# Kernel tuning notes

Measured on AMD Instinct MI355X. Metric: run time of the kernel, lower is better.

The kernel has to match this reference:

```python
import jax, jax.numpy as jnp
import numpy as np

FEAT, HW, C, M, U, B = 2048, 14, 20, 64, 128, 4


def _grid_sample_one(img, grid):
    # img: [M, H, W]; grid: [H, W, 2] normalized coords (x, y), align_corners=True, zero padding
    H, W = img.shape[-2], img.shape[-1]
    gx = (grid[..., 0] + 1.0) * 0.5 * (W - 1)
    gy = (grid[..., 1] + 1.0) * 0.5 * (H - 1)
    x0 = jnp.floor(gx).astype(jnp.int32); x1 = x0 + 1
    y0 = jnp.floor(gy).astype(jnp.int32); y1 = y0 + 1

    def gather(yi, xi):
        valid = (yi >= 0) & (yi < H) & (xi >= 0) & (xi < W)
        yc = jnp.clip(yi, 0, H - 1); xc = jnp.clip(xi, 0, W - 1)
        return img[:, yc, xc] * valid.astype(img.dtype)  # [M, H, W]

    w00 = (x1 - gx) * (y1 - gy); w01 = (gx - x0) * (y1 - gy)
    w10 = (x1 - gx) * (gy - y0); w11 = (gx - x0) * (gy - y0)
    return (gather(y0, x0) * w00 + gather(y0, x1) * w01 +
            gather(y1, x0) * w10 + gather(y1, x1) * w11)


def setup_inputs() -> dict:
    key = jax.random.key(0)
    ks = jax.random.split(key, 5)
    x = jax.random.normal(ks[0], (B, FEAT, HW, HW), jnp.float32)
    W_parcel = jax.random.normal(ks[1], (C, M, FEAT), jnp.float32) * 0.02
    W_stn = jax.random.normal(ks[2], (C, 6, M * (HW // 2) ** 2), jnp.float32) * 1e-3
    b_stn = jnp.tile(jnp.array([1.0, 0.0, 0.0, 0.0, 1.0, 0.0], jnp.float32), (C, 1))
    Wg = jax.random.normal(ks[3], (C, C - 1, U, 2 * M), jnp.float32) * 0.02
    w_phi = jax.random.normal(ks[4], (1, U), jnp.float32) * 0.05
    b_phi = jnp.zeros((1,), jnp.float32)
    return {"x": x, "W_parcel": W_parcel, "W_stn": W_stn, "b_stn": b_stn,
            "Wg": Wg, "w_phi": w_phi, "b_phi": b_phi}


def reference(x, W_parcel, W_stn, b_stn, Wg, w_phi, b_phi):
    b, _, H, W = x.shape
    # per-class 1x1 conv parcels: [B, C, M, H, W]
    x_tmp = jnp.einsum('bfhw,cmf->bcmhw', x, W_parcel)
    # relu + 2x2 maxpool -> [B, C, M, 7, 7]
    pooled = jax.nn.relu(x_tmp).reshape(b, C, M, H // 2, 2, W // 2, 2).max(axis=(4, 6))
    flat = pooled.reshape(b, C, M * (H // 2) * (W // 2))
    theta = (jnp.einsum('bck,cjk->bcj', flat, W_stn) + b_stn).reshape(b, C, 2, 3)
    # affine grid (align_corners=True): base[h, w] = [x_norm, y_norm, 1]
    xs = jnp.linspace(-1.0, 1.0, W); ys = jnp.linspace(-1.0, 1.0, H)
    base = jnp.stack(jnp.broadcast_arrays(xs[None, :], ys[:, None], jnp.ones((H, W))), -1)
    grid = jnp.einsum('bcij,hwj->bchwi', theta, base)  # [B, C, H, W, 2]
    # STN sampling of the pre-relu parcel maps
    x_obj = jax.vmap(jax.vmap(_grid_sample_one))(x_tmp, grid)  # [B, C, M, H, W]
    # pairwise relation: relu(Wa[i,j] x_obj[i] + Wb[i,j] x_obj[j]) summed over j != i
    jidx = jnp.asarray(np.array([[k for k in range(C) if k != c] for c in range(C)]))
    Wa, Wb = Wg[..., :M], Wg[..., M:]
    A = jnp.einsum('ckum,bcmhw->bckuhw', Wa, x_obj)
    Bp = jnp.einsum('ckum,bckmhw->bckuhw', Wb, x_obj[:, jidx])
    rel = jax.nn.relu(A + Bp).sum(axis=2)          # [B, C, U, H, W]
    rel_mean = rel.mean(axis=(-2, -1))             # [B, C, U]  (adaptive avg pool 1x1)
    out = jnp.einsum('bcu,ou->bco', rel_mean, w_phi)[..., 0] + b_phi  # [B, C]
    return out
```

## Files before the change

kernel.cpp:

```cpp
#include <hip/hip_runtime.h>

#define FEAT 2048
#define HWD 14
#define NPIX 196
#define C_CLS 20
#define M_DIM 64
#define U_DIM 128
#define B_SZ 4
#define K_REL 19
#define NPOOL 49

typedef __attribute__((ext_vector_type(8))) short bf16x8s;
typedef __attribute__((ext_vector_type(8))) unsigned short ushort8v;
typedef __attribute__((ext_vector_type(4))) float f32x4;
typedef __attribute__((ext_vector_type(4))) unsigned int uint4v;

__device__ inline unsigned short f2bf(float f) {
    unsigned u = __builtin_bit_cast(unsigned, f);
    unsigned r = (u + 0x7FFF + ((u >> 16) & 1)) >> 16;
    return (unsigned short)r;
}

__global__ __launch_bounds__(256) void prep_kernel(
        const float* __restrict__ x, const float* __restrict__ Wp,
        const float* __restrict__ Wg,
        unsigned short* __restrict__ xts, unsigned short* __restrict__ Awp,
        unsigned short* __restrict__ Awg) {
    __shared__ unsigned short SM[128 * 136];
    const int blk = blockIdx.x;
    const int tid = threadIdx.x;
    const int lane = tid & 63, wv = tid >> 6;
    const int l15 = lane & 15, lq = lane >> 4;

    if (blk < 128) {
        unsigned short (*T)[210] = (unsigned short (*)[210])SM;
        const int b = blk >> 5;
        const int s = blk & 31;
        const float* xb = x + ((size_t)b * FEAT + s * 64) * NPIX;
        for (int i = tid; i < 64 * NPIX; i += 256) {
            int kk = i / NPIX, hw = i - kk * NPIX;
            T[kk][hw] = f2bf(xb[(size_t)kk * NPIX + hw]);
        }
        __syncthreads();
        unsigned short* ob = xts + ((size_t)(b * 32 + s)) * 1664 * 8;
        for (int i = tid; i < 1664; i += 256) {
            int ch = i / 208, row = i - ch * 208;
            ushort8v o;
#pragma unroll
            for (int j = 0; j < 8; j++)
                o[j] = (row < NPIX) ? T[ch * 8 + j][row] : (unsigned short)0;
            *(ushort8v*)(ob + (size_t)i * 8) = o;
        }
    } else if (blk < 288) {
        unsigned short (*TP)[264] = (unsigned short (*)[264])SM;
        const int p = blk - 128;
        const int c = p >> 3, kc = p & 7;
        const float* wsrc = Wp + ((size_t)c * M_DIM) * FEAT + kc * 256;
#pragma unroll
        for (int it = 0; it < 16; it++) {
            int i4 = tid + it * 256;
            int m = i4 >> 6, c4 = i4 & 63;
            float4 v = *(const float4*)(wsrc + (size_t)m * FEAT + c4 * 4);
            TP[m][c4 * 4 + 0] = f2bf(v.x);
            TP[m][c4 * 4 + 1] = f2bf(v.y);
            TP[m][c4 * 4 + 2] = f2bf(v.z);
            TP[m][c4 * 4 + 3] = f2bf(v.w);
        }
        __syncthreads();
#pragma unroll
        for (int fr = 0; fr < 8; fr++) {
            int ss = wv;
            int fi = fr;
            int rt = fi >> 1, f = fi & 1;
            int m = rt * 16 + l15;
            int kl = ss * 64 + f * 32 + lq * 8;
            bf16x8s vfrag = *(const bf16x8s*)(&TP[m][kl]);
            int s = kc * 4 + ss;
            *(bf16x8s*)(Awp + (((size_t)(c * 32 + s) * 8 + fi) * 64 + lane) * 8) = vfrag;
        }
    } else {
        unsigned short (*TG)[136] = (unsigned short (*)[136])SM;
        const int ck = blk - 288;
        const float* gsrc = Wg + (size_t)ck * U_DIM * 128;
#pragma unroll
        for (int it = 0; it < 16; it++) {
            int i4 = tid + it * 256;
            int u = i4 >> 5, c4 = i4 & 31;
            float4 v = *(const float4*)(gsrc + (size_t)u * 128 + c4 * 4);
            TG[u][c4 * 4 + 0] = f2bf(v.x);
            TG[u][c4 * 4 + 1] = f2bf(v.y);
            TG[u][c4 * 4 + 2] = f2bf(v.z);
            TG[u][c4 * 4 + 3] = f2bf(v.w);
        }
        __syncthreads();
#pragma unroll
        for (int fr = 0; fr < 8; fr++) {
            int fi = fr;
            int ut = fi >> 2, ks = fi & 3;
            int u = wv * 32 + ut * 16 + l15;
            int mm = ks * 32 + lq * 8;
            bf16x8s vfrag = *(const bf16x8s*)(&TG[u][mm]);
            *(bf16x8s*)(Awg + (((size_t)(ck * 4 + wv) * 8 + fi) * 64 + lane) * 8) = vfrag;
        }
    }
}

__global__ __launch_bounds__(512) void gemmphase_kernel(
        const unsigned short* __restrict__ xts,
        const unsigned short* __restrict__ Awp,
        const float* __restrict__ Wstn,
        const float* __restrict__ bstn,
        unsigned short* __restrict__ x_objT) {
    __shared__ __align__(16) char smem[78336];
    float* xs     = (float*)smem;
    float* pooled = (float*)(smem + 53504);
    float* red    = (float*)(smem + 66048);

    const int c = blockIdx.x, b = blockIdx.y;
    const int tid = threadIdx.x;
    const int lane = tid & 63, wv = tid >> 6;
    const int l15 = lane & 15, lq = lane >> 4;
    const int kh = wv >> 2;
    const int cg = wv & 3;
    const int t0 = (cg == 0) ? 0 : (3 * cg + 1);
    const int nt = (cg == 0) ? 4 : 3;

    const unsigned short* xsrc = xts + (size_t)b * 32 * 1664 * 8;
    const unsigned short* asrc = Awp + (size_t)c * 256 * 64 * 8;
    const int s0 = kh * 16;

    bf16x8s A0[8], A1[8], B0[8], B1[8];
    auto aload = [&](int s, bf16x8s (&A)[8]) {
#pragma unroll
        for (int fi = 0; fi < 8; fi++)
            A[fi] = *(const bf16x8s*)(asrc + (((size_t)s * 8 + fi) * 64 + lane) * 8);
    };
    auto bload = [&](int s, bf16x8s (&B)[8]) {
#pragma unroll
        for (int q = 0; q < 4; q++) {
            if (q < nt) {
#pragma unroll
                for (int f = 0; f < 2; f++)
                    B[q * 2 + f] = *(const bf16x8s*)(xsrc +
                        ((size_t)s * 1664 + (f * 4 + lq) * 208 + (t0 + q) * 16 + l15) * 8);
            }
        }
    };

    f32x4 acc[4][4];
#pragma unroll
    for (int q = 0; q < 4; q++)
#pragma unroll
        for (int rt = 0; rt < 4; rt++) acc[q][rt] = (f32x4){0.f, 0.f, 0.f, 0.f};

    auto compute = [&](bf16x8s (&A)[8], bf16x8s (&B)[8]) {
#pragma unroll
        for (int q = 0; q < 4; q++) {
            if (q < nt) {
#pragma unroll
                for (int rt = 0; rt < 4; rt++)
#pragma unroll
                    for (int f = 0; f < 2; f++)
                        acc[q][rt] = __builtin_amdgcn_mfma_f32_16x16x32_bf16(
                            A[rt * 2 + f], B[q * 2 + f], acc[q][rt], 0, 0, 0);
            }
        }
    };

    aload(s0, A0); bload(s0, B0);
#pragma unroll
    for (int sp = 0; sp < 8; sp++) {
        aload(s0 + 2 * sp + 1, A1); bload(s0 + 2 * sp + 1, B1);
        compute(A0, B0);
        if (sp < 7) { aload(s0 + 2 * sp + 2, A0); bload(s0 + 2 * sp + 2, B0); }
        compute(A1, B1);
    }

    if (kh == 0) {
#pragma unroll
        for (int q = 0; q < 4; q++) {
            if (q < nt) {
                int tt = t0 + q;
#pragma unroll
                for (int rt = 0; rt < 4; rt++)
#pragma unroll
                    for (int r = 0; r < 4; r++)
                        xs[(rt * 16 + lq * 4 + r) * 209 + tt * 16 + l15] = acc[q][rt][r];
            }
        }
    }
    __syncthreads();
    if (kh == 1) {
#pragma unroll
        for (int q = 0; q < 4; q++) {
            if (q < nt) {
                int tt = t0 + q;
#pragma unroll
                for (int rt = 0; rt < 4; rt++)
#pragma unroll
                    for (int r = 0; r < 4; r++)
                        xs[(rt * 16 + lq * 4 + r) * 209 + tt * 16 + l15] += acc[q][rt][r];
            }
        }
    }
    __syncthreads();

    for (int i = tid; i < 3136; i += 512) {
        int m = i / NPOOL, p = i - m * NPOOL;
        int ph = p / 7, pw = p - ph * 7;
        const float* bp = &xs[m * 209 + ph * 2 * HWD + pw * 2];
        float v = fmaxf(fmaxf(bp[0], bp[1]), fmaxf(bp[HWD], bp[HWD + 1]));
        pooled[i] = fmaxf(v, 0.f);
    }
    __syncthreads();

    float sj[6] = {0, 0, 0, 0, 0, 0};
#pragma unroll
    for (int it = 0; it < 7; it++) {
        int kk = tid + it * 512;
        if (kk < 3136) {
            float f = pooled[kk];
#pragma unroll
            for (int j = 0; j < 6; j++)
                sj[j] += f * Wstn[((size_t)c * 6 + j) * 3136 + kk];
        }
    }
#pragma unroll
    for (int j = 0; j < 6; j++) red[j * 512 + tid] = sj[j];
    __syncthreads();
    for (int off = 256; off > 0; off >>= 1) {
        if (tid < off) {
#pragma unroll
            for (int j = 0; j < 6; j++)
                red[j * 512 + tid] += red[j * 512 + tid + off];
        }
        __syncthreads();
    }
    float th[6];
#pragma unroll
    for (int j = 0; j < 6; j++) th[j] = red[j * 512] + bstn[c * 6 + j];

    unsigned short* obase = x_objT + ((size_t)(b * C_CLS + c) * 208) * 64;
    for (int i = tid; i < 12 * 64; i += 512)
        obase[(size_t)(NPIX + i / 64) * 64 + (i & 63)] = 0;

    const int m = tid & 63;
    const int hwg = tid >> 6;
    unsigned short* ob = obase + m;
    const float* xrow = &xs[m * 209];
    for (int it = 0; it < 25; it++) {
        int hw = hwg + it * 8;
        if (hw >= NPIX) break;
        int h = hw / HWD, w = hw - h * HWD;
        float fx = -1.f + w * (2.f / 13.f);
        float fy = -1.f + h * (2.f / 13.f);
        float gxn = th[0] * fx + th[1] * fy + th[2];
        float gyn = th[3] * fx + th[4] * fy + th[5];
        float gx = (gxn + 1.f) * 0.5f * (HWD - 1);
        float gy = (gyn + 1.f) * 0.5f * (HWD - 1);
        float x0f = floorf(gx), y0f = floorf(gy);
        int x0 = (int)x0f, y0 = (int)y0f;
        int x1 = x0 + 1, y1 = y0 + 1;
        auto gat = [&](int yi, int xi) -> float {
            bool v = (yi >= 0) & (yi < HWD) & (xi >= 0) & (xi < HWD);
            int yc = min(max(yi, 0), HWD - 1);
            int xc = min(max(xi, 0), HWD - 1);
            return v ? xrow[yc * HWD + xc] : 0.f;
        };
        float xw1 = (float)x1 - gx, xw0 = gx - (float)x0;
        float yw1 = (float)y1 - gy, yw0 = gy - (float)y0;
        float val = gat(y0, x0) * xw1 * yw1 + gat(y0, x1) * xw0 * yw1 +
                    gat(y1, x0) * xw1 * yw0 + gat(y1, x1) * xw0 * yw0;
        ob[(size_t)hw * 64] = f2bf(val);
    }
}

#define MP 136
__global__ __launch_bounds__(256) void relation_mfma_kernel(
        const unsigned short* __restrict__ x_objT,
        const unsigned short* __restrict__ Awg,
        float* __restrict__ partial) {
    __shared__ unsigned short Xs[208 * MP];
    const int k = blockIdx.x;
    const int c = blockIdx.y;
    const int b = blockIdx.z;
    const int kj = (k < c) ? k : k + 1;
    const int tid = threadIdx.x;
    const int lane = tid & 63;
    const int wv = tid >> 6;
    const int l15 = lane & 15;
    const int lq = lane >> 4;

    bf16x8s AF[2][4];
    const unsigned short* ab = Awg + (((size_t)(c * K_REL + k) * 4 + wv) * 8 * 64) * 8;
#pragma unroll
    for (int ut = 0; ut < 2; ut++)
#pragma unroll
        for (int ks = 0; ks < 4; ks++)
            AF[ut][ks] = *(const bf16x8s*)(ab + ((size_t)(ut * 4 + ks) * 64 + lane) * 8);

    const unsigned short* xc = x_objT + ((size_t)(b * C_CLS + c)) * 208 * 64;
    const unsigned short* xk = x_objT + ((size_t)(b * C_CLS + kj)) * 208 * 64;
#pragma unroll
    for (int it = 0; it < 13; it++) {
        int i = tid + it * 256;
        int hw = i >> 4, ch = i & 15;
        const unsigned short* src = (ch < 8 ? xc : xk) + (size_t)hw * 64 + (ch & 7) * 8;
        *(uint4v*)(&Xs[hw * MP + ch * 8]) = *(const uint4v*)src;
    }
    __syncthreads();

    float csum[2][4];
#pragma unroll
    for (int ut = 0; ut < 2; ut++)
#pragma unroll
        for (int r = 0; r < 4; r++) csum[ut][r] = 0.f;

    for (int t = 0; t < 13; t++) {
        bf16x8s BF[4];
#pragma unroll
        for (int ks = 0; ks < 4; ks++)
            BF[ks] = *(const bf16x8s*)(&Xs[(t * 16 + l15) * MP + ks * 32 + lq * 8]);
        f32x4 acc0 = {0.f, 0.f, 0.f, 0.f}, acc1 = {0.f, 0.f, 0.f, 0.f};
#pragma unroll
        for (int ks = 0; ks < 4; ks++) {
            acc0 = __builtin_amdgcn_mfma_f32_16x16x32_bf16(AF[0][ks], BF[ks], acc0, 0, 0, 0);
            acc1 = __builtin_amdgcn_mfma_f32_16x16x32_bf16(AF[1][ks], BF[ks], acc1, 0, 0, 0);
        }
#pragma unroll
        for (int r = 0; r < 4; r++) {
            csum[0][r] += fmaxf(acc0[r], 0.f);
            csum[1][r] += fmaxf(acc1[r], 0.f);
        }
    }
#pragma unroll
    for (int mask = 1; mask < 16; mask <<= 1) {
#pragma unroll
        for (int ut = 0; ut < 2; ut++)
#pragma unroll
            for (int r = 0; r < 4; r++)
                csum[ut][r] += __shfl_xor(csum[ut][r], mask, 64);
    }
    if (l15 == 0) {
        float* pp = partial + (((size_t)b * C_CLS + c) * K_REL + k) * U_DIM;
#pragma unroll
        for (int ut = 0; ut < 2; ut++)
#pragma unroll
            for (int r = 0; r < 4; r++)
                pp[wv * 32 + ut * 16 + lq * 4 + r] = csum[ut][r];
    }
}

__global__ __launch_bounds__(128) void final_kernel(
        const float* __restrict__ partial, const float* __restrict__ wphi,
        const float* __restrict__ bphi, float* __restrict__ out) {
    int bc = blockIdx.x;
    int u = threadIdx.x;
    float s = 0.f;
    for (int k = 0; k < K_REL; k++)
        s += partial[((size_t)bc * K_REL + k) * U_DIM + u];
    s *= wphi[u];
    __shared__ float red[128];
    red[u] = s;
    __syncthreads();
    for (int off = 64; off > 0; off >>= 1) {
        if (u < off) red[u] += red[u + off];
        __syncthreads();
    }
    if (u == 0) out[bc] = red[0] / (float)NPIX + bphi[0];
}

extern "C" void kernel_launch(void* const* d_in, const int* in_sizes, int n_in,
                              void* d_out, int out_size, void* d_ws, size_t ws_size,
                              hipStream_t stream) {
    const float* x    = (const float*)d_in[0];
    const float* Wp   = (const float*)d_in[1];
    const float* Wstn = (const float*)d_in[2];
    const float* bstn = (const float*)d_in[3];
    const float* Wg   = (const float*)d_in[4];
    const float* wphi = (const float*)d_in[5];
    const float* bphi = (const float*)d_in[6];
    float* out = (float*)d_out;
    char* wsb = (char*)d_ws;

    unsigned short* xts    = (unsigned short*)(wsb);
    unsigned short* Awp    = (unsigned short*)(wsb + 3407872);
    unsigned short* Awg    = (unsigned short*)(wsb + 8650752);
    unsigned short* x_objT = (unsigned short*)(wsb + 21102592);
    float* partial         = (float*)(wsb + 23232512);

    prep_kernel<<<668, 256, 0, stream>>>(x, Wp, Wg, xts, Awp, Awg);
    gemmphase_kernel<<<dim3(C_CLS, B_SZ), 512, 0, stream>>>(xts, Awp, Wstn, bstn, x_objT);
    relation_mfma_kernel<<<dim3(K_REL, C_CLS, B_SZ), 256, 0, stream>>>(x_objT, Awg, partial);
    final_kernel<<<80, 128, 0, stream>>>(partial, wphi, bphi, out);
}
```

Measured before the change: 65.02 us.

## Fuse final reduction into relation kernel via last-block atomic counter; swizzle block ids

Removes the separate final_kernel launch. Each relation block bumps a per-(b,c) atomic counter, and the last block to finish sums the partials and writes the output. Counters are zeroed in prep_kernel. Block indices in the gemmphase and relation kernels are remapped with an XCD-style swizzle (stride 8) so related work lands on the same chiplet and shares L2. This adds threadfence and atomic overhead and a small serial tail in the last block.

Result: slower. 194.6 us (+199.4%).

```diff
diff --git a/kernel.cpp b/kernel.cpp
--- a/kernel.cpp
+++ b/kernel.cpp
@@ -25,12 +25,14 @@
         const float* __restrict__ x, const float* __restrict__ Wp,
         const float* __restrict__ Wg,
         unsigned short* __restrict__ xts, unsigned short* __restrict__ Awp,
-        unsigned short* __restrict__ Awg) {
+        unsigned short* __restrict__ Awg, int* __restrict__ cnt) {
     __shared__ unsigned short SM[128 * 136];
     const int blk = blockIdx.x;
     const int tid = threadIdx.x;
     const int lane = tid & 63, wv = tid >> 6;
     const int l15 = lane & 15, lq = lane >> 4;
+
+    if (blk == 0 && tid < 80) cnt[tid] = 0;
 
     if (blk < 128) {
         unsigned short (*T)[210] = (unsigned short (*)[210])SM;
@@ -116,7 +118,8 @@
     float* pooled = (float*)(smem + 53504);
     float* red    = (float*)(smem + 66048);
 
-    const int c = blockIdx.x, b = blockIdx.y;
+    const int flat = (blockIdx.x & 7) * 10 + (blockIdx.x >> 3);
+    const int c = flat % C_CLS, b = flat / C_CLS;
     const int tid = threadIdx.x;
     const int lane = tid & 63, wv = tid >> 6;
     const int l15 = lane & 15, lq = lane >> 4;
@@ -279,11 +282,17 @@
 __global__ __launch_bounds__(256) void relation_mfma_kernel(
         const unsigned short* __restrict__ x_objT,
         const unsigned short* __restrict__ Awg,
-        float* __restrict__ partial) {
+        float* __restrict__ partial,
+        const float* __restrict__ wphi, const float* __restrict__ bphi,
+        int* __restrict__ cnt, float* __restrict__ out) {
     __shared__ unsigned short Xs[208 * MP];
-    const int k = blockIdx.x;
-    const int c = blockIdx.y;
-    const int b = blockIdx.z;
+    __shared__ int lastFlag;
+    __shared__ float redf[128];
+    const int swz = (blockIdx.x & 7) * 190 + (blockIdx.x >> 3);
+    const int k = swz % K_REL;
+    const int bc = swz / K_REL;
+    const int c = bc % C_CLS;
+    const int b = bc / C_CLS;
     const int kj = (k < c) ? k : k + 1;
     const int tid = threadIdx.x;
     const int lane = tid & 63;
@@ -342,32 +351,36 @@
                 csum[ut][r] += __shfl_xor(csum[ut][r], mask, 64);
     }
     if (l15 == 0) {
-        float* pp = partial + (((size_t)b * C_CLS + c) * K_REL + k) * U_DIM;
+        float* pp = partial + ((size_t)bc * K_REL + k) * U_DIM;
 #pragma unroll
         for (int ut = 0; ut < 2; ut++)
 #pragma unroll
             for (int r = 0; r < 4; r++)
                 pp[wv * 32 + ut * 16 + lq * 4 + r] = csum[ut][r];
     }
-}
-
-__global__ __launch_bounds__(128) void final_kernel(
-        const float* __restrict__ partial, const float* __restrict__ wphi,
-        const float* __restrict__ bphi, float* __restrict__ out) {
-    int bc = blockIdx.x;
-    int u = threadIdx.x;
-    float s = 0.f;
-    for (int k = 0; k < K_REL; k++)
-        s += partial[((size_t)bc * K_REL + k) * U_DIM + u];
-    s *= wphi[u];
-    __shared__ float red[128];
-    red[u] = s;
-    __syncthreads();
-    for (int off = 64; off > 0; off >>= 1) {
-        if (u < off) red[u] += red[u + off];
+
+    __threadfence();
+    if (tid == 0) {
+        int old = atomicAdd(&cnt[bc], 1);
+        lastFlag = (old == K_REL - 1);
+    }
+    __syncthreads();
+    if (lastFlag) {
+        __threadfence();
+        float s = 0.f;
+        if (tid < U_DIM) {
+            const float* pp = partial + (size_t)bc * K_REL * U_DIM + tid;
+            for (int k2 = 0; k2 < K_REL; k2++) s += pp[(size_t)k2 * U_DIM];
+            s *= wphi[tid];
+        }
+        if (tid < 128) redf[tid] = s;
         __syncthreads();
-    }
-    if (u == 0) out[bc] = red[0] / (float)NPIX + bphi[0];
+        for (int off = 64; off > 0; off >>= 1) {
+            if (tid < off) redf[tid] += redf[tid + off];
+            __syncthreads();
+        }
+        if (tid == 0) out[bc] = redf[0] / (float)NPIX + bphi[0];
+    }
 }
 
 extern "C" void kernel_launch(void* const* d_in, const int* in_sizes, int n_in,
@@ -388,9 +401,10 @@
     unsigned short* Awg    = (unsigned short*)(wsb + 8650752);
     unsigned short* x_objT = (unsigned short*)(wsb + 21102592);
     float* partial         = (float*)(wsb + 23232512);
-
-    prep_kernel<<<668, 256, 0, stream>>>(x, Wp, Wg, xts, Awp, Awg);
-    gemmphase_kernel<<<dim3(C_CLS, B_SZ), 512, 0, stream>>>(xts, Awp, Wstn, bstn, x_objT);
-    relation_mfma_kernel<<<dim3(K_REL, C_CLS, B_SZ), 256, 0, stream>>>(x_objT, Awg, partial);
-    final_kernel<<<80, 128, 0, stream>>>(partial, wphi, bphi, out);
+    int* cnt               = (int*)(wsb + 24010752);
+
+    prep_kernel<<<668, 256, 0, stream>>>(x, Wp, Wg, xts, Awp, Awg, cnt);
+    gemmphase_kernel<<<80, 512, 0, stream>>>(xts, Awp, Wstn, bstn, x_objT);
+    relation_mfma_kernel<<<1520, 256, 0, stream>>>(x_objT, Awg, partial,
+                                                   wphi, bphi, cnt, out);
 }
```
